# Kernel optimization log

Measured on AMD Instinct MI355X. Metric: run time of the kernel, lower is better.

## Reference

```python
import jax, jax.numpy as jnp
import numpy as np

N_HEADS = 16
HEAD_SZ = 64

def setup_inputs() -> dict:
    key = jax.random.key(0)
    ks = jax.random.split(key, 6)
    E = 1024
    s = 1.0 / np.sqrt(E)
    return {
        "x": jax.random.normal(ks[0], (2, 2048, E), dtype=jnp.float32),
        "Wq": jax.random.normal(ks[1], (E, N_HEADS * HEAD_SZ), dtype=jnp.float32) * s,
        "Wk": jax.random.normal(ks[2], (E, N_HEADS * HEAD_SZ), dtype=jnp.float32) * s,
        "Wv": jax.random.normal(ks[3], (E, N_HEADS * HEAD_SZ), dtype=jnp.float32) * s,
        "Wp": jax.random.normal(ks[4], (N_HEADS * HEAD_SZ, E), dtype=jnp.float32) * s,
        "bp": jnp.zeros((E,), dtype=jnp.float32),
    }

def reference(x, Wq, Wk, Wv, Wp, bp):
    # flavor="masked": causal self-attention, pdrop=0 -> dropout is identity
    B, S, E = x.shape
    H, D = N_HEADS, HEAD_SZ
    q = (x @ Wq).reshape(B, S, H, D).transpose(0, 2, 1, 3)  # [B,H,S,D]
    k = (x @ Wk).reshape(B, S, H, D).transpose(0, 2, 1, 3)
    v = (x @ Wv).reshape(B, S, H, D).transpose(0, 2, 1, 3)
    scores = jnp.einsum("bhqd,bhkd->bhqk", q, k) / jnp.sqrt(jnp.float32(D))
    causal = jnp.tril(jnp.ones((S, S), dtype=bool))  # [S,S]
    scores = jnp.where(causal, scores, -jnp.inf)
    attn = jax.nn.softmax(scores, axis=-1)
    out = jnp.einsum("bhqk,bhkd->bhqd", attn, v)  # [B,H,S,D]
    out = out.transpose(0, 2, 1, 3).reshape(B, S, H * D)
    return out @ Wp + bp
```

## Files before the change

kernel.cpp:

```cpp
#include <hip/hip_runtime.h>
#include <hip/hip_bf16.h>
#include <math.h>

using bf16 = __hip_bfloat16;
typedef __attribute__((ext_vector_type(8))) short short8;
typedef __attribute__((ext_vector_type(4))) float floatx4;

#define MFMA16(a, b, c) __builtin_amdgcn_mfma_f32_16x16x32_bf16((a), (b), (c), 0, 0, 0)

__device__ __forceinline__ void gll16(const void* g, void* l) {
  __builtin_amdgcn_global_load_lds((__attribute__((address_space(1))) void*)(uintptr_t)g,
                                   (__attribute__((address_space(3))) void*)l, 16, 0, 0);
}

__global__ void detect_bias_k(const unsigned short* __restrict__ x,
                              const void* __restrict__ bsrc,
                              bf16* __restrict__ bdst, int* __restrict__ flag) {
  __shared__ int cnt;
  if (threadIdx.x == 0) cnt = 0;
  __syncthreads();
  int local = 0;
  for (int i = threadIdx.x; i < 8192; i += 256) {
    unsigned short v = x[2 * i];
    if (((v >> 7) & 0xFF) == 0xFF) local++;
  }
  if (local) atomicAdd(&cnt, local);
  __syncthreads();
  int f = (cnt > 0) ? 1 : 0;
  if (threadIdx.x == 0) *flag = f;
  for (int i = threadIdx.x; i < 1024; i += 256)
    bdst[i] = f ? __float2bfloat16(((const float*)bsrc)[i]) : ((const bf16*)bsrc)[i];
}

__global__ __launch_bounds__(256) void prep_k(const void* __restrict__ xin,
                                              bf16* __restrict__ xb,
                                              const void* __restrict__ W0,
                                              const void* __restrict__ W1,
                                              const void* __restrict__ W2,
                                              const void* __restrict__ W3,
                                              bf16* __restrict__ Wt,
                                              bf16* __restrict__ Wpt,
                                              const int* __restrict__ flag) {
  bool f32 = (*flag != 0);
  int z = blockIdx.z;
  if (z < 2) {
    int tid = threadIdx.y * 32 + threadIdx.x;
    int blockLin = z * 1024 + blockIdx.y * 32 + blockIdx.x;
    int idx = blockLin * 2048 + tid * 8;
    if (f32) {
      const float4* p = reinterpret_cast<const float4*>((const float*)xin + idx);
      float4 a = p[0], b = p[1];
      union { bf16 h[8]; uint4 u; } U;
      U.h[0] = __float2bfloat16(a.x); U.h[1] = __float2bfloat16(a.y);
      U.h[2] = __float2bfloat16(a.z); U.h[3] = __float2bfloat16(a.w);
      U.h[4] = __float2bfloat16(b.x); U.h[5] = __float2bfloat16(b.y);
      U.h[6] = __float2bfloat16(b.z); U.h[7] = __float2bfloat16(b.w);
      *reinterpret_cast<uint4*>(xb + idx) = U.u;
    } else {
      *reinterpret_cast<uint4*>(xb + idx) =
          *reinterpret_cast<const uint4*>((const bf16*)xin + idx);
    }
    return;
  }
  const void* src = (z == 2) ? W0 : (z == 3) ? W1 : (z == 4) ? W2 : W3;
  bf16* dst = (z == 5) ? Wpt : (Wt + (size_t)(z - 2) * 1024 * 1024);
  __shared__ float tsh[32][33];
  int tx = threadIdx.x, ty = threadIdx.y;
  int k0 = blockIdx.y * 32, n0 = blockIdx.x * 32;
  for (int i = 0; i < 4; i++) {
    size_t off = (size_t)(k0 + ty + i * 8) * 1024 + n0 + tx;
    tsh[ty + i * 8][tx] = f32 ? ((const float*)src)[off]
                              : __bfloat162float(((const bf16*)src)[off]);
  }
  __syncthreads();
  for (int i = 0; i < 4; i++)
    dst[(size_t)(n0 + ty + i * 8) * 1024 + k0 + tx] = __float2bfloat16(tsh[tx][ty + i * 8]);
}

__global__ __launch_bounds__(512) void vtrans_k(const bf16* __restrict__ QKV,
                                                bf16* __restrict__ VT) {
  __shared__ bf16 t[64][66];
  int tx = threadIdx.x, ty = threadIdx.y;
  int s0 = blockIdx.x * 64, bh = blockIdx.y;
  int b = bh >> 4, h = bh & 15;
  size_t rowb = (size_t)b * 2048;
  int hv = 2048 + h * 64;
#pragma unroll
  for (int i = 0; i < 8; i++)
    t[i * 8 + ty][tx] = QKV[(rowb + s0 + i * 8 + ty) * 3072 + hv + tx];
  __syncthreads();
#pragma unroll
  for (int i = 0; i < 8; i++)
    VT[((size_t)bh * 64 + i * 8 + ty) * 2048 + s0 + tx] = t[tx][i * 8 + ty];
}

__global__ __launch_bounds__(256) void gemm_bt128(const bf16* __restrict__ A, int lda,
                                                  const bf16* __restrict__ Bt, int ldb,
                                                  void* __restrict__ C, int ldc,
                                                  const bf16* __restrict__ bias, int K,
                                                  const int* __restrict__ outflag) {
  __shared__ bf16 As[2][128 * 32];
  __shared__ bf16 Bs[2][128 * 32];
  int t = threadIdx.x;
  int w = t >> 6, lane = t & 63;
  int g = lane >> 4, c = lane & 15;
  int wm = (w >> 1) * 64, wn = (w & 1) * 64;
  int m0 = blockIdx.y * 128, n0 = blockIdx.x * 128;

  int sr = w * 32 + (lane >> 2);
  int sc = (lane & 3) * 8;
  const bf16* Ab = A + (size_t)(m0 + sr) * lda + sc;
  const bf16* Bb = Bt + (size_t)(n0 + sr) * ldb + sc;
  int lofs = (w * 32) * 32;

  floatx4 acc[4][4] = {};

  for (int k0 = 0; k0 < K; k0 += 64) {
    __syncthreads();
#pragma unroll
    for (int h = 0; h < 2; h++) {
      gll16(Ab + k0 + h * 32, &As[h][lofs]);
      gll16(Ab + k0 + h * 32 + (size_t)16 * lda, &As[h][lofs + 16 * 32]);
      gll16(Bb + k0 + h * 32, &Bs[h][lofs]);
      gll16(Bb + k0 + h * 32 + (size_t)16 * ldb, &Bs[h][lofs + 16 * 32]);
    }
    __syncthreads();
#pragma unroll
    for (int h = 0; h < 2; h++) {
      short8 af[4], bf[4];
#pragma unroll
      for (int i = 0; i < 4; i++) {
        af[i] = *reinterpret_cast<const short8*>(&As[h][(wm + i * 16 + c) * 32 + g * 8]);
        bf[i] = *reinterpret_cast<const short8*>(&Bs[h][(wn + i * 16 + c) * 32 + g * 8]);
      }
#pragma unroll
      for (int i = 0; i < 4; i++)
#pragma unroll
        for (int j = 0; j < 4; j++) acc[i][j] = MFMA16(af[i], bf[j], acc[i][j]);
    }
  }

  bool f32out = (outflag != nullptr) && (*outflag != 0);
#pragma unroll
  for (int i = 0; i < 4; i++) {
    int rbase = m0 + wm + i * 16 + g * 4;
#pragma unroll
    for (int j = 0; j < 4; j++) {
      int col = n0 + wn + j * 16 + c;
      float bv = bias ? __bfloat162float(bias[col]) : 0.f;
#pragma unroll
      for (int r = 0; r < 4; r++) {
        size_t off = (size_t)(rbase + r) * ldc + col;
        float v = acc[i][j][r] + bv;
        if (f32out) ((float*)C)[off] = v;
        else ((bf16*)C)[off] = __float2bfloat16(v);
      }
    }
  }
}

__global__ __launch_bounds__(256) void gemm_bt64(const bf16* __restrict__ A, int lda,
                                                 const bf16* __restrict__ Bt, int ldb,
                                                 void* __restrict__ C, int ldc,
                                                 const bf16* __restrict__ bias, int K,
                                                 const int* __restrict__ outflag) {
  __shared__ bf16 As[2][128 * 32];
  __shared__ bf16 Bs[2][64 * 32];
  int t = threadIdx.x;
  int w = t >> 6, lane = t & 63;
  int g = lane >> 4, c = lane & 15;
  int wm = (w >> 1) * 64, wn = (w & 1) * 32;
  int m0 = blockIdx.y * 128, n0 = blockIdx.x * 64;

  int sr = (lane >> 2);
  int sc = (lane & 3) * 8;
  const bf16* Ab = A + (size_t)(m0 + w * 32 + sr) * lda + sc;
  const bf16* Bb = Bt + (size_t)(n0 + w * 16 + sr) * ldb + sc;
  int laofs = (w * 32) * 32;
  int lbofs = (w * 16) * 32;

  floatx4 acc[4][2] = {};

  for (int k0 = 0; k0 < K; k0 += 64) {
    __syncthreads();
#pragma unroll
    for (int h = 0; h < 2; h++) {
      gll16(Ab + k0 + h * 32, &As[h][laofs]);
      gll16(Ab + k0 + h * 32 + (size_t)16 * lda, &As[h][laofs + 16 * 32]);
      gll16(Bb + k0 + h * 32, &Bs[h][lbofs]);
    }
    __syncthreads();
#pragma unroll
    for (int h = 0; h < 2; h++) {
      short8 af[4], bf[2];
#pragma unroll
      for (int i = 0; i < 4; i++)
        af[i] = *reinterpret_cast<const short8*>(&As[h][(wm + i * 16 + c) * 32 + g * 8]);
#pragma unroll
      for (int j = 0; j < 2; j++)
        bf[j] = *reinterpret_cast<const short8*>(&Bs[h][(wn + j * 16 + c) * 32 + g * 8]);
#pragma unroll
      for (int i = 0; i < 4; i++)
#pragma unroll
        for (int j = 0; j < 2; j++) acc[i][j] = MFMA16(af[i], bf[j], acc[i][j]);
    }
  }

  bool f32out = (outflag != nullptr) && (*outflag != 0);
#pragma unroll
  for (int i = 0; i < 4; i++) {
    int rbase = m0 + wm + i * 16 + g * 4;
#pragma unroll
    for (int j = 0; j < 2; j++) {
      int col = n0 + wn + j * 16 + c;
      float bv = bias ? __bfloat162float(bias[col]) : 0.f;
#pragma unroll
      for (int r = 0; r < 4; r++) {
        size_t off = (size_t)(rbase + r) * ldc + col;
        float v = acc[i][j][r] + bv;
        if (f32out) ((float*)C)[off] = v;
        else ((bf16*)C)[off] = __float2bfloat16(v);
      }
    }
  }
}

__device__ const int QT_TAB[8][3] = {{15, 15, 0}, {7, 13, 1},  {14, 12, 2}, {14, 10, 3},
                                     {13, 4, 9},  {6, 10, 8},  {12, 11, 8}, {5, 11, 9}};
__device__ const int HF_TAB[8][3] = {{0, 1, 2}, {2, 0, 2}, {0, 0, 2}, {1, 0, 2},
                                     {1, 2, 0}, {2, 1, 0}, {1, 0, 1}, {2, 1, 1}};

__global__ __launch_bounds__(512, 4) void attn_lds2(bf16* __restrict__ QKV,
                                                    const bf16* __restrict__ VT,
                                                    float* __restrict__ Po,
                                                    float* __restrict__ Pl) {
  const int S = 2048, LD = 3072;
  __shared__ bf16 Ks[2][2][64 * 32];
  __shared__ bf16 Vs[2][2][64 * 32];
  __shared__ bf16 Pb[8][16 * 72];

  int t = threadIdx.x, w = t >> 6, lane = t & 63, g = lane >> 4, c = lane & 15;

  int r = blockIdx.x + 24 * blockIdx.y;
  int xcd = r & 7;
  int s = r >> 3;
  int r3 = s >> 5;
  int u = s & 31;
  int hg = u >> 3;
  int tri = u & 7;
  int bh = xcd + 8 * hg;
  int qt = QT_TAB[tri][r3];
  int hf = HF_TAB[tri][r3];

  int b = bh >> 4, h = bh & 15;
  int qbase = qt * 128;
  size_t rowb = (size_t)b * S;
  int hq = h * 64, hk = 1024 + h * 64;
  const bf16* Vt = VT + (size_t)bh * 64 * 2048;
  bf16* pb = Pb[w];

  int nkt = 2 * qt + 2;
  int kb0 = (hf == 1) ? (qt + 1) : 0;
  int kb1 = (hf == 0) ? (qt + 1) : nkt;

  int su = (w & 3) * 16 + (lane >> 2);
  int sc = (lane & 3) * 8;
  const bf16* Kg = &QKV[(rowb + su) * LD + hk + sc];
  const bf16* Vg = &Vt[(size_t)su * 2048 + sc];
  int sofs = ((w & 3) * 16) * 32;

  short8 qf[2];
#pragma unroll
  for (int hfr = 0; hfr < 2; hfr++)
    qf[hfr] = *reinterpret_cast<const short8*>(
        &QKV[(rowb + qbase + w * 16 + c) * LD + hq + hfr * 32 + g * 8]);

  floatx4 o[4] = {};
  float lsum = 0.f;
  int qrow = qbase + w * 16 + c;

  {
    size_t k0off = (size_t)kb0 * 64;
    if (w < 4) {
      gll16(Kg + k0off * LD, &Ks[0][0][sofs]);
      gll16(Kg + k0off * LD + 32, &Ks[0][1][sofs]);
    } else {
      gll16(Vg + k0off, &Vs[0][0][sofs]);
      gll16(Vg + k0off + 32, &Vs[0][1][sofs]);
    }
  }

  for (int kt = kb0; kt < kb1; kt++) {
    int kbase = kt * 64;
    int cur = (kt - kb0) & 1;
    __syncthreads();
    if (kt + 1 < kb1) {
      int nb = cur ^ 1;
      size_t kofs = (size_t)(kbase + 64);
      if (w < 4) {
        gll16(Kg + kofs * LD, &Ks[nb][0][sofs]);
        gll16(Kg + kofs * LD + 32, &Ks[nb][1][sofs]);
      } else {
        gll16(Vg + kofs, &Vs[nb][0][sofs]);
        gll16(Vg + kofs + 32, &Vs[nb][1][sofs]);
      }
    }

    short8 kf[4][2];
#pragma unroll
    for (int nt = 0; nt < 4; nt++)
#pragma unroll
      for (int hfr = 0; hfr < 2; hfr++)
        kf[nt][hfr] =
            *reinterpret_cast<const short8*>(&Ks[cur][hfr][(nt * 16 + c) * 32 + g * 8]);

    floatx4 sv[4];
    __builtin_amdgcn_s_setprio(1);
#pragma unroll
    for (int nt = 0; nt < 4; nt++) {
      floatx4 z = {};
      z = MFMA16(kf[nt][0], qf[0], z);
      z = MFMA16(kf[nt][1], qf[1], z);
      sv[nt] = z;
    }
    __builtin_amdgcn_s_setprio(0);

    bool diag = (kbase + 63 > qbase + w * 16);
#pragma unroll
    for (int nt = 0; nt < 4; nt++) {
      int kcol0 = kbase + nt * 16 + g * 4;
#pragma unroll
      for (int rr = 0; rr < 4; rr++) {
        float arg = fmaf(sv[nt][rr], 0.18033688f, -23.083120f);
        if (diag && (kcol0 + rr > qrow)) arg = -1e30f;
        float p = exp2f(arg);
        lsum += p;
        sv[nt][rr] = p;
      }
    }

#pragma unroll
    for (int nt = 0; nt < 4; nt++) {
      union { bf16 h4[4]; uint2 u2; } U;
      U.h4[0] = __float2bfloat16(sv[nt][0]);
      U.h4[1] = __float2bfloat16(sv[nt][1]);
      U.h4[2] = __float2bfloat16(sv[nt][2]);
      U.h4[3] = __float2bfloat16(sv[nt][3]);
      *reinterpret_cast<uint2*>(&pb[c * 72 + nt * 16 + g * 4]) = U.u2;
    }
    asm volatile("s_waitcnt lgkmcnt(0)" ::: "memory");
    short8 pf0 = *reinterpret_cast<const short8*>(&pb[c * 72 + g * 8]);
    short8 pf1 = *reinterpret_cast<const short8*>(&pb[c * 72 + 32 + g * 8]);

    __builtin_amdgcn_s_setprio(1);
#pragma unroll
    for (int dt = 0; dt < 4; dt++) {
      short8 vf0 = *reinterpret_cast<const short8*>(&Vs[cur][0][(dt * 16 + c) * 32 + g * 8]);
      short8 vf1 = *reinterpret_cast<const short8*>(&Vs[cur][1][(dt * 16 + c) * 32 + g * 8]);
      o[dt] = MFMA16(pf0, vf0, o[dt]);
      o[dt] = MFMA16(pf1, vf1, o[dt]);
    }
    __builtin_amdgcn_s_setprio(0);
  }

  lsum += __shfl_xor(lsum, 16);
  lsum += __shfl_xor(lsum, 32);

  if (hf == 2) {
    float lrec = 1.0f / lsum;
    float l_r[4];
#pragma unroll
    for (int rr = 0; rr < 4; rr++) l_r[rr] = __shfl(lrec, g * 4 + rr);
#pragma unroll
    for (int dt = 0; dt < 4; dt++)
#pragma unroll
      for (int rr = 0; rr < 4; rr++) {
        float v = o[dt][rr] * l_r[rr];
        QKV[(rowb + qbase + w * 16 + g * 4 + rr) * LD + hq + dt * 16 + c] =
            __float2bfloat16(v);
      }
  } else {
    int slot = (bh * 8 + (qt - 8)) * 2 + hf;
    float* po = Po + (size_t)slot * (128 * 64);
    float* pl = Pl + slot * 128;
    if (g == 0) pl[w * 16 + c] = lsum;
#pragma unroll
    for (int dt = 0; dt < 4; dt++)
#pragma unroll
      for (int rr = 0; rr < 4; rr++)
        po[(w * 16 + g * 4 + rr) * 64 + dt * 16 + c] = o[dt][rr];
  }
}

__global__ __launch_bounds__(256) void combine_k(const float* __restrict__ Po,
                                                 const float* __restrict__ Pl,
                                                 bf16* __restrict__ QKV) {
  int qi = blockIdx.x;
  int bh = blockIdx.y;
  int b = bh >> 4, h = bh & 15;
  int qt = 8 + qi;
  int slot = (bh * 8 + qi) * 2;
  const float* oA = Po + (size_t)slot * (128 * 64);
  const float* oB = oA + 128 * 64;
  const float* lA = Pl + slot * 128;
  const float* lB = lA + 128;
  int t = threadIdx.x;
#pragma unroll
  for (int i = 0; i < 32; i++) {
    int idx = t + i * 256;
    int row = idx >> 6, d = idx & 63;
    float l = lA[row] + lB[row];
    float v = (oA[idx] + oB[idx]) / l;
    QKV[((size_t)b * 2048 + qt * 128 + row) * 3072 + h * 64 + d] = __float2bfloat16(v);
  }
}

extern "C" void kernel_launch(void* const* d_in, const int* in_sizes, int n_in,
                              void* d_out, int out_size, void* d_ws, size_t ws_size,
                              hipStream_t stream) {
  char* ws = (char*)d_ws;
  const size_t MB = 1024 * 1024;
  int* flag = (int*)ws;
  bf16* bias = (bf16*)(ws + 4096);
  bf16* xb = (bf16*)(ws + 1 * MB);
  bf16* Wt = (bf16*)(ws + 9 * MB);
  bf16* Wpt = (bf16*)(ws + 15 * MB);
  bf16* QKV = (bf16*)(ws + 17 * MB);
  bf16* VT = xb;
  float* Pl = (float*)(ws + 41 * MB);
  float* Po = (out_size >= (int)(16 * MB)) ? (float*)d_out
                                           : (float*)(ws + 42 * MB);

  detect_bias_k<<<1, 256, 0, stream>>>((const unsigned short*)d_in[0], d_in[5], bias, flag);
  prep_k<<<dim3(32, 32, 6), dim3(32, 8), 0, stream>>>(d_in[0], xb, d_in[1], d_in[2],
                                                      d_in[3], d_in[4], Wt, Wpt, flag);

  gemm_bt128<<<dim3(24, 32), 256, 0, stream>>>(xb, 1024, Wt, 1024, QKV, 3072, nullptr,
                                               1024, nullptr);
  vtrans_k<<<dim3(32, 32), dim3(64, 8), 0, stream>>>(QKV, VT);
  attn_lds2<<<dim3(24, 32), 512, 0, stream>>>(QKV, VT, Po, Pl);
  combine_k<<<dim3(8, 32), 256, 0, stream>>>(Po, Pl, QKV);
  gemm_bt64<<<dim3(16, 32), 256, 0, stream>>>(QKV, 3072, Wpt, 1024, d_out, 1024, bias,
                                              1024, flag);
}
```

Before: 197.6 us.

## Double-buffer GEMM K-loop with prefetch and split diagonal masking in attention

Both projection GEMM kernels move from a load-then-compute loop over 64-wide K chunks to a double-buffered pipeline over 32-wide K chunks. The next tile is fetched into LDS with global_load_lds while the current one is computed, which leaves one barrier per step instead of two, and MFMA priority is raised during compute. The staging layout changes so each wave loads 16 rows at offsets 0 and 64. Separately, the attention softmax now splits off non-diagonal tiles into a branch with no mask check. The risk is that a single barrier per iteration may not fully protect the buffer being overwritten, and there are more loop iterations.

```diff
diff --git a/kernel.cpp b/kernel.cpp
--- a/kernel.cpp
+++ b/kernel.cpp
@@ -107,38 +107,56 @@
   int wm = (w >> 1) * 64, wn = (w & 1) * 64;
   int m0 = blockIdx.y * 128, n0 = blockIdx.x * 128;
 
-  int sr = w * 32 + (lane >> 2);
+  int sr = w * 16 + (lane >> 2);
   int sc = (lane & 3) * 8;
   const bf16* Ab = A + (size_t)(m0 + sr) * lda + sc;
   const bf16* Bb = Bt + (size_t)(n0 + sr) * ldb + sc;
-  int lofs = (w * 32) * 32;
+  int lofs = (w * 16) * 32;
+
+#define STG128(d, kk)                                                 \
+  {                                                                   \
+    gll16(Ab + (kk), &As[d][lofs]);                                   \
+    gll16(Ab + (kk) + (size_t)64 * lda, &As[d][lofs + 64 * 32]);      \
+    gll16(Bb + (kk), &Bs[d][lofs]);                                   \
+    gll16(Bb + (kk) + (size_t)64 * ldb, &Bs[d][lofs + 64 * 32]);      \
+  }
 
   floatx4 acc[4][4] = {};
-
-  for (int k0 = 0; k0 < K; k0 += 64) {
+  int nsteps = K >> 5;
+
+  STG128(0, 0);
+  __syncthreads();
+  int cur = 0;
+  for (int s = 0; s < nsteps - 1; ++s) {
+    STG128(cur ^ 1, (s + 1) * 32);
+    short8 af[4], bf[4];
+#pragma unroll
+    for (int i = 0; i < 4; i++) {
+      af[i] = *reinterpret_cast<const short8*>(&As[cur][(wm + i * 16 + c) * 32 + g * 8]);
+      bf[i] = *reinterpret_cast<const short8*>(&Bs[cur][(wn + i * 16 + c) * 32 + g * 8]);
+    }
+    __builtin_amdgcn_s_setprio(1);
+#pragma unroll
+    for (int i = 0; i < 4; i++)
+#pragma unroll
+      for (int j = 0; j < 4; j++) acc[i][j] = MFMA16(af[i], bf[j], acc[i][j]);
+    __builtin_amdgcn_s_setprio(0);
     __syncthreads();
-#pragma unroll
-    for (int h = 0; h < 2; h++) {
-      gll16(Ab + k0 + h * 32, &As[h][lofs]);
-      gll16(Ab + k0 + h * 32 + (size_t)16 * lda, &As[h][lofs + 16 * 32]);
-      gll16(Bb + k0 + h * 32, &Bs[h][lofs]);
-      gll16(Bb + k0 + h * 32 + (size_t)16 * ldb, &Bs[h][lofs + 16 * 32]);
-    }
-    __syncthreads();
-#pragma unroll
-    for (int h = 0; h < 2; h++) {
-      short8 af[4], bf[4];
-#pragma unroll
-      for (int i = 0; i < 4; i++) {
-        af[i] = *reinterpret_cast<const short8*>(&As[h][(wm + i * 16 + c) * 32 + g * 8]);
-        bf[i] = *reinterpret_cast<const short8*>(&Bs[h][(wn + i * 16 + c) * 32 + g * 8]);
-      }
-#pragma unroll
-      for (int i = 0; i < 4; i++)
-#pragma unroll
-        for (int j = 0; j < 4; j++) acc[i][j] = MFMA16(af[i], bf[j], acc[i][j]);
-    }
-  }
+    cur ^= 1;
+  }
+  {
+    short8 af[4], bf[4];
+#pragma unroll
+    for (int i = 0; i < 4; i++) {
+      af[i] = *reinterpret_cast<const short8*>(&As[cur][(wm + i * 16 + c) * 32 + g * 8]);
+      bf[i] = *reinterpret_cast<const short8*>(&Bs[cur][(wn + i * 16 + c) * 32 + g * 8]);
+    }
+#pragma unroll
+    for (int i = 0; i < 4; i++)
+#pragma unroll
+      for (int j = 0; j < 4; j++) acc[i][j] = MFMA16(af[i], bf[j], acc[i][j]);
+  }
+#undef STG128
 
   bool f32out = (outflag != nullptr) && (*outflag != 0);
 #pragma unroll
@@ -172,39 +190,57 @@
   int wm = (w >> 1) * 64, wn = (w & 1) * 32;
   int m0 = blockIdx.y * 128, n0 = blockIdx.x * 64;
 
-  int sr = (lane >> 2);
+  int sr = w * 16 + (lane >> 2);
   int sc = (lane & 3) * 8;
-  const bf16* Ab = A + (size_t)(m0 + w * 32 + sr) * lda + sc;
-  const bf16* Bb = Bt + (size_t)(n0 + w * 16 + sr) * ldb + sc;
-  int laofs = (w * 32) * 32;
-  int lbofs = (w * 16) * 32;
+  const bf16* Ab = A + (size_t)(m0 + sr) * lda + sc;
+  const bf16* Bb = Bt + (size_t)(n0 + sr) * ldb + sc;
+  int lofs = (w * 16) * 32;
+
+#define STG64(d, kk)                                                  \
+  {                                                                   \
+    gll16(Ab + (kk), &As[d][lofs]);                                   \
+    gll16(Ab + (kk) + (size_t)64 * lda, &As[d][lofs + 64 * 32]);      \
+    gll16(Bb + (kk), &Bs[d][lofs]);                                   \
+  }
 
   floatx4 acc[4][2] = {};
-
-  for (int k0 = 0; k0 < K; k0 += 64) {
+  int nsteps = K >> 5;
+
+  STG64(0, 0);
+  __syncthreads();
+  int cur = 0;
+  for (int s = 0; s < nsteps - 1; ++s) {
+    STG64(cur ^ 1, (s + 1) * 32);
+    short8 af[4], bf[2];
+#pragma unroll
+    for (int i = 0; i < 4; i++)
+      af[i] = *reinterpret_cast<const short8*>(&As[cur][(wm + i * 16 + c) * 32 + g * 8]);
+#pragma unroll
+    for (int j = 0; j < 2; j++)
+      bf[j] = *reinterpret_cast<const short8*>(&Bs[cur][(wn + j * 16 + c) * 32 + g * 8]);
+    __builtin_amdgcn_s_setprio(1);
+#pragma unroll
+    for (int i = 0; i < 4; i++)
+#pragma unroll
+      for (int j = 0; j < 2; j++) acc[i][j] = MFMA16(af[i], bf[j], acc[i][j]);
+    __builtin_amdgcn_s_setprio(0);
     __syncthreads();
-#pragma unroll
-    for (int h = 0; h < 2; h++) {
-      gll16(Ab + k0 + h * 32, &As[h][laofs]);
-      gll16(Ab + k0 + h * 32 + (size_t)16 * lda, &As[h][laofs + 16 * 32]);
-      gll16(Bb + k0 + h * 32, &Bs[h][lbofs]);
-    }
-    __syncthreads();
-#pragma unroll
-    for (int h = 0; h < 2; h++) {
-      short8 af[4], bf[2];
-#pragma unroll
-      for (int i = 0; i < 4; i++)
-        af[i] = *reinterpret_cast<const short8*>(&As[h][(wm + i * 16 + c) * 32 + g * 8]);
-#pragma unroll
-      for (int j = 0; j < 2; j++)
-        bf[j] = *reinterpret_cast<const short8*>(&Bs[h][(wn + j * 16 + c) * 32 + g * 8]);
-#pragma unroll
-      for (int i = 0; i < 4; i++)
-#pragma unroll
-        for (int j = 0; j < 2; j++) acc[i][j] = MFMA16(af[i], bf[j], acc[i][j]);
-    }
-  }
+    cur ^= 1;
+  }
+  {
+    short8 af[4], bf[2];
+#pragma unroll
+    for (int i = 0; i < 4; i++)
+      af[i] = *reinterpret_cast<const short8*>(&As[cur][(wm + i * 16 + c) * 32 + g * 8]);
+#pragma unroll
+    for (int j = 0; j < 2; j++)
+      bf[j] = *reinterpret_cast<const short8*>(&Bs[cur][(wn + j * 16 + c) * 32 + g * 8]);
+#pragma unroll
+    for (int i = 0; i < 4; i++)
+#pragma unroll
+      for (int j = 0; j < 2; j++) acc[i][j] = MFMA16(af[i], bf[j], acc[i][j]);
+  }
+#undef STG64
 
   bool f32out = (outflag != nullptr) && (*outflag != 0);
 #pragma unroll
@@ -326,16 +362,27 @@
     __builtin_amdgcn_s_setprio(0);
 
     bool diag = (kbase + 63 > qbase + w * 16);
-#pragma unroll
-    for (int nt = 0; nt < 4; nt++) {
-      int kcol0 = kbase + nt * 16 + g * 4;
-#pragma unroll
-      for (int rr = 0; rr < 4; rr++) {
-        float arg = fmaf(sv[nt][rr], 0.18033688f, -23.083120f);
-        if (diag && (kcol0 + rr > qrow)) arg = -1e30f;
-        float p = exp2f(arg);
-        lsum += p;
-        sv[nt][rr] = p;
+    if (!diag) {
+#pragma unroll
+      for (int nt = 0; nt < 4; nt++)
+#pragma unroll
+        for (int rr = 0; rr < 4; rr++) {
+          float p = exp2f(fmaf(sv[nt][rr], 0.18033688f, -23.083120f));
+          lsum += p;
+          sv[nt][rr] = p;
+        }
+    } else {
+#pragma unroll
+      for (int nt = 0; nt < 4; nt++) {
+        int kcol0 = kbase + nt * 16 + g * 4;
+#pragma unroll
+        for (int rr = 0; rr < 4; rr++) {
+          float arg = fmaf(sv[nt][rr], 0.18033688f, -23.083120f);
+          if (kcol0 + rr > qrow) arg = -1e30f;
+          float p = exp2f(arg);
+          lsum += p;
+          sv[nt][rr] = p;
+        }
       }
     }
 
```

After: 210.4 us. 1.06x slower.
